# Optimization experiments

Hardware: AMD Instinct MI355X
Metric: run time of the kernel (lower is better)

Reference implementation:

```python
import jax, jax.numpy as jnp
import numpy as np

B, C, H, W = 2, 64, 256, 256
DW = 128          # c * DW_Expand
FFN = 128         # c * FFN_Expand
GRID = 8          # wH = wW modulation grid


def setup_inputs() -> dict:
    key = jax.random.key(0)
    ks = jax.random.split(key, 16)
    rn = lambda k, s, sc=1.0: jax.random.normal(k, s, jnp.float32) * sc
    return {
        "x": rn(ks[0], (B, C, H, W)),
        "w1": rn(ks[1], (DW, C), (2.0 / C) ** 0.5),
        "b1": jnp.zeros((DW,), jnp.float32),
        "w2": rn(ks[2], (DW, 3, 3), (2.0 / 9.0) ** 0.5),
        "b2": jnp.zeros((DW,), jnp.float32),
        "w3": rn(ks[3], (C, DW // 2), (2.0 / (DW // 2)) ** 0.5),
        "b3": jnp.zeros((C,), jnp.float32),
        "sca_w": rn(ks[4], (DW // 2, DW // 2), (1.0 / (DW // 2)) ** 0.5),
        "sca_b": jnp.zeros((DW // 2,), jnp.float32),
        "w4": rn(ks[5], (FFN, C), (2.0 / C) ** 0.5),
        "b4": jnp.zeros((FFN,), jnp.float32),
        "w5": rn(ks[6], (C, FFN // 2), (2.0 / (FFN // 2)) ** 0.5),
        "b5": jnp.zeros((C,), jnp.float32),
        "n1_w": jnp.ones((C,), jnp.float32),
        "n1_b": jnp.zeros((C,), jnp.float32),
        "n2_w": jnp.ones((C,), jnp.float32),
        "n2_b": jnp.zeros((C,), jnp.float32),
        "beta": rn(ks[7], (C,), 0.1),
        "gamma": rn(ks[8], (C,), 0.1),
        "mod1": rn(ks[9], (B, DW, C, GRID, GRID)),
        "mod2": rn(ks[10], (B, DW, GRID, GRID)),
        "mod3": rn(ks[11], (B, C, DW // 2, GRID, GRID)),
        "mod4": rn(ks[12], (B, FFN, C, GRID, GRID)),
        "mod5": rn(ks[13], (B, C, FFN // 2, GRID, GRID)),
    }


def layernorm2d(x, w, b, eps=1e-6):
    # channel-wise LayerNorm per pixel (NAFNet LayerNorm2d)
    mu = jnp.mean(x, axis=1, keepdims=True)
    var = jnp.mean((x - mu) ** 2, axis=1, keepdims=True)
    return (x - mu) / jnp.sqrt(var + eps) * w[None, :, None, None] + b[None, :, None, None]


def conv1x1_modulated(x, wb, bb, mod):
    # wb: [Co,Ci], mod: [B,Co,Ci,wH,wW]; per-patch 1x1 conv with normalized dynamic weights
    w = wb[None, :, :, None, None] * mod                      # [B,Co,Ci,wH,wW]
    w = w / jnp.sqrt(jnp.sum(w * w, axis=2, keepdims=True))   # normalize over Ci (kh*kw==1)
    b_, ci, h, wd = x.shape
    wh, ww = mod.shape[-2:]
    ph, pw = h // wh, wd // ww
    xp = x.reshape(b_, ci, wh, ph, ww, pw)                    # split into patches
    y = jnp.einsum('bocuv,bcupvq->boupvq', w, xp)             # per-patch matmul
    return y.reshape(b_, wb.shape[0], h, wd) + bb[None, :, None, None]


def conv3x3_dw_modulated(x, wb, bb, mod):
    # wb: [C,3,3], mod: [B,C,wH,wW]; per-patch depthwise 3x3, padding 1 across whole image
    w = wb[None, :, :, :, None, None] * mod[:, :, None, None, :, :]  # [B,C,3,3,wH,wW]
    w = w / jnp.sqrt(jnp.sum(w * w, axis=(2, 3), keepdims=True))     # normalize over (ci=1, kh*kw)
    b_, c, h, wd = x.shape
    wh, ww = mod.shape[-2:]
    ph, pw = h // wh, wd // ww
    xpad = jnp.pad(x, ((0, 0), (0, 0), (1, 1), (1, 1)))
    out = jnp.zeros_like(x)
    for dh in range(3):
        for dw_ in range(3):
            xs = xpad[:, :, dh:dh + h, dw_:dw_ + wd].reshape(b_, c, wh, ph, ww, pw)
            wk = w[:, :, dh, dw_, :, :]                        # [B,C,wH,wW]
            out = out + (wk[:, :, :, None, :, None] * xs).reshape(b_, c, h, wd)
    return out + bb[None, :, None, None]


def simple_gate(x):
    a, g = jnp.split(x, 2, axis=1)
    return a * g


def reference(x, w1, b1, w2, b2, w3, b3, sca_w, sca_b, w4, b4, w5, b5,
              n1_w, n1_b, n2_w, n2_b, beta, gamma, mod1, mod2, mod3, mod4, mod5):
    y = layernorm2d(x, n1_w, n1_b)
    y = conv1x1_modulated(y, w1, b1, mod1)
    y = conv3x3_dw_modulated(y, w2, b2, mod2)
    y = simple_gate(y)
    s = jnp.mean(y, axis=(2, 3), keepdims=True)               # SCA: global pool + 1x1
    s = jnp.einsum('oc,bcij->boij', sca_w, s) + sca_b[None, :, None, None]
    y = y * s
    y = conv1x1_modulated(y, w3, b3, mod3)
    y1 = x + y * beta[None, :, None, None]
    z = conv1x1_modulated(layernorm2d(y1, n2_w, n2_b), w4, b4, mod4)
    z = simple_gate(z)
    z = conv1x1_modulated(z, w5, b5, mod5)
    return y1 + z * gamma[None, :, None, None]
```

## Files before the change

kernel.cpp:

```cpp
#include <hip/hip_runtime.h>
#include <hip/hip_bf16.h>


typedef __bf16 bf16x8 __attribute__((ext_vector_type(8)));
typedef float f32x4 __attribute__((ext_vector_type(4)));
typedef unsigned short u16x8 __attribute__((ext_vector_type(8)));

__device__ __forceinline__ float b2f(unsigned short u) {
    union { unsigned int i; float f; } x; x.i = ((unsigned int)u) << 16; return x.f;
}
__device__ __forceinline__ unsigned short f2b(float f) {
    union { float f; unsigned int i; } x; x.f = f;
    unsigned int i = x.i;
    return (unsigned short)((i + 0x7FFFu + ((i >> 16) & 1u)) >> 16);
}
__device__ __forceinline__ unsigned int pk2(float a, float b) {
    __hip_bfloat162 h = __float22bfloat162_rn(float2{a, b});
    union { __hip_bfloat162 h; unsigned int u; } cv; cv.h = h; return cv.u;
}

__global__ __launch_bounds__(256) void prep_k(
    const float* __restrict__ w1, const float* __restrict__ mod1,
    const float* __restrict__ w3, const float* __restrict__ mod3,
    const float* __restrict__ beta,
    const float* __restrict__ w4, const float* __restrict__ mod4,
    const float* __restrict__ w5, const float* __restrict__ mod5,
    const float* __restrict__ gam,
    unsigned short* __restrict__ pw1, unsigned short* __restrict__ pw3,
    unsigned short* __restrict__ pw4, unsigned short* __restrict__ pw5)
{
    const int tid = threadIdx.x;
    int blk = blockIdx.x;
    const float* w; const float* mod; const float* rows = nullptr;
    unsigned short* out; int NOUT; int rem;
    if (blk < 256)      { w = w1; mod = mod1; out = pw1; NOUT = 128; rem = blk; }
    else if (blk < 384) { w = w3; mod = mod3; out = pw3; NOUT = 64;  rem = blk - 256; rows = beta; }
    else if (blk < 640) { w = w4; mod = mod4; out = pw4; NOUT = 128; rem = blk - 384; }
    else                { w = w5; mod = mod5; out = pw5; NOUT = 64;  rem = blk - 640; rows = gam; }
    const int b = rem / NOUT, o = rem % NOUT;

    __shared__ float mlds[64 * 68];
    __shared__ float wlsh[64];
    __shared__ float red[4 * 64];
    __shared__ float rs[64];

    const float* mbase = mod + ((size_t)(b * NOUT + o) * 64) * 64;
#pragma unroll
    for (int k = 0; k < 4; ++k) {
        int l = tid + k * 256;
        float4 vv = ((const float4*)mbase)[l];
        int c = l >> 4, q = l & 15;
        *(float4*)&mlds[c * 68 + q * 4] = vv;
    }
    if (tid < 64) wlsh[tid] = w[o * 64 + tid];
    __syncthreads();

    {
        int uv = tid & 63, part = tid >> 6;
        float ss = 0.f;
#pragma unroll
        for (int j = 0; j < 16; ++j) {
            int c = part * 16 + j;
            float t = wlsh[c] * mlds[c * 68 + uv];
            ss += t * t;
        }
        red[part * 64 + uv] = ss;
    }
    __syncthreads();
    if (tid < 64) {
        float tot = red[tid] + red[64 + tid] + red[128 + tid] + red[192 + tid];
        float rv = rows ? rows[tid == tid ? o : o] : 1.f;
        rs[tid] = rsqrtf(fmaxf(tot, 1e-30f)) * (rows ? rows[o] : 1.f) * (rv == rv ? 1.f : 1.f);
    }
    __syncthreads();

    {
        int uvw = tid >> 2, cp = tid & 3;
        float r = rs[uvw];
        size_t obase = ((size_t)(b * 64 + uvw) * NOUT + o) * 64;
#pragma unroll
        for (int g = 0; g < 2; ++g) {
            u16x8 pk;
#pragma unroll
            for (int e = 0; e < 8; ++e) {
                int c = cp * 16 + g * 8 + e;
                pk[e] = f2b(wlsh[c] * mlds[c * 68 + uvw] * r);
            }
            *(u16x8*)&out[obase + cp * 16 + g * 8] = pk;
        }
    }
}

__global__ __launch_bounds__(256, 2) void head_k(
    const float* __restrict__ x, unsigned short* __restrict__ t1,
    const unsigned short* __restrict__ pw1, const float* __restrict__ b1,
    const float* __restrict__ n1w, const float* __restrict__ n1b, int bbase)
{
    const int tid   = threadIdx.x;
    const int chunk = blockIdx.x;
    const int uv    = blockIdx.y;
    const int z     = blockIdx.z;
    const int bfull = z + bbase;
    const int u = uv >> 3, v = uv & 7;
    const int h_base = u * 32 + chunk * 4;
    const int w_base = v * 32;

    __shared__ __align__(16) unsigned short stage[128 * 72];

    const int wave = tid >> 6;
    const int lane = tid & 63;
    const int q = lane >> 4;
    const int r = lane & 15;
    const int nfi[2] = {2 * wave, 2 * wave + 1};

    const unsigned short* pwt = pw1 + ((size_t)(bfull * 64 + uv) * 128) * 64;
    bf16x8 bfr[2][2];
#pragma unroll
    for (int f = 0; f < 2; ++f)
#pragma unroll
        for (int ks = 0; ks < 2; ++ks)
            bfr[f][ks] = *(const bf16x8*)&pwt[(16 * nfi[f] + r) * 64 + ks * 32 + q * 8];
    float bsc[2] = {b1[16 * nfi[0] + r], b1[16 * nfi[1] + r]};

    const int cg = tid & 7;
    const int qd = tid >> 3;
    const int c0 = cg * 8;
    const int pixg = (h_base + (qd >> 3)) * 256 + w_base + (qd & 7) * 4;
    float v2[8][4];
#pragma unroll
    for (int k = 0; k < 8; ++k) {
        float4 t = *(const float4*)&x[((z * 64 + c0 + k) << 16) + pixg];
        v2[k][0] = t.x; v2[k][1] = t.y; v2[k][2] = t.z; v2[k][3] = t.w;
    }
    float lw[8], lb[8];
    *(float4*)&lw[0] = *(const float4*)&n1w[c0];
    *(float4*)&lw[4] = *(const float4*)&n1w[c0 + 4];
    *(float4*)&lb[0] = *(const float4*)&n1b[c0];
    *(float4*)&lb[4] = *(const float4*)&n1b[c0 + 4];
#pragma unroll
    for (int e = 0; e < 4; ++e) {
        float s1 = 0.f, s2 = 0.f;
#pragma unroll
        for (int k = 0; k < 8; ++k) { s1 += v2[k][e]; s2 += v2[k][e] * v2[k][e]; }
#pragma unroll
        for (int m = 1; m < 8; m <<= 1) { s1 += __shfl_xor(s1, m); s2 += __shfl_xor(s2, m); }
        float mu = s1 * (1.f / 64.f);
        float var = s2 * (1.f / 64.f) - mu * mu;
        float rstd = rsqrtf(fmaxf(var, 0.f) + 1e-6f);
        float o8[8];
#pragma unroll
        for (int k = 0; k < 8; ++k) o8[k] = (v2[k][e] - mu) * rstd * lw[k] + lb[k];
        uint4 pk;
        pk.x = pk2(o8[0], o8[1]); pk.y = pk2(o8[2], o8[3]);
        pk.z = pk2(o8[4], o8[5]); pk.w = pk2(o8[6], o8[7]);
        *(uint4*)&stage[(qd * 4 + e) * 72 + c0] = pk;
    }

    __syncthreads();

    f32x4 acc[8][2];
#pragma unroll
    for (int mi = 0; mi < 8; ++mi) { acc[mi][0] = (f32x4){0,0,0,0}; acc[mi][1] = (f32x4){0,0,0,0}; }
#pragma unroll
    for (int mi = 0; mi < 8; ++mi) {
        bf16x8 a0 = *(const bf16x8*)&stage[(16 * mi + r) * 72 + q * 8];
        bf16x8 a1 = *(const bf16x8*)&stage[(16 * mi + r) * 72 + 32 + q * 8];
#pragma unroll
        for (int f = 0; f < 2; ++f) {
            acc[mi][f] = __builtin_amdgcn_mfma_f32_16x16x32_bf16(a0, bfr[f][0], acc[mi][f], 0, 0, 0);
            acc[mi][f] = __builtin_amdgcn_mfma_f32_16x16x32_bf16(a1, bfr[f][1], acc[mi][f], 0, 0, 0);
        }
    }

#pragma unroll
    for (int mi = 0; mi < 8; ++mi) {
        int lp0 = 16 * mi + 4 * q;
        int pix = (h_base + (lp0 >> 5)) * 256 + w_base + (lp0 & 31);
#pragma unroll
        for (int f = 0; f < 2; ++f) {
            int o = 16 * nfi[f] + r;
            float bs = bsc[f];
            *(uint2*)&t1[((z * 128 + o) << 16) + pix] =
                make_uint2(pk2(acc[mi][f][0] + bs, acc[mi][f][1] + bs),
                           pk2(acc[mi][f][2] + bs, acc[mi][f][3] + bs));
        }
    }
}

__global__ __launch_bounds__(256, 2) void tail_k(
    const unsigned short* __restrict__ t3, const float* __restrict__ x,
    float* __restrict__ outp,
    const unsigned short* __restrict__ pw3, const float* __restrict__ b3,
    const float* __restrict__ beta,
    const unsigned short* __restrict__ pw4, const float* __restrict__ b4,
    const float* __restrict__ n2w, const float* __restrict__ n2b,
    const unsigned short* __restrict__ pw5, const float* __restrict__ b5,
    const float* __restrict__ gam,
    const float* __restrict__ svec, int bbase)
{
    const int tid   = threadIdx.x;
    const int chunk = blockIdx.x;
    const int uv    = blockIdx.y;
    const int z     = blockIdx.z;
    const int bfull = z + bbase;
    const int u = uv >> 3, v = uv & 7;
    const int h_base = u * 32 + chunk * 4;
    const int w_base = v * 32;

    __shared__ __align__(16) unsigned short stage[128 * 72];

    const int wave = tid >> 6;
    const int lane = tid & 63;
    const int q = lane >> 4;
    const int r = lane & 15;
    const int oo = 16 * wave + r;

    const unsigned short* p3 = pw3 + (size_t)(bfull * 64 + uv) * 64 * 64;
    const unsigned short* p4 = pw4 + (size_t)(bfull * 64 + uv) * 128 * 64;
    const unsigned short* p5 = pw5 + (size_t)(bfull * 64 + uv) * 64 * 64;
    bf16x8 w3f[2], w5f[2], w4f[2][2];
    const int nfi4[2] = {wave, wave + 4};
#pragma unroll
    for (int ks = 0; ks < 2; ++ks) {
        w3f[ks] = *(const bf16x8*)&p3[(oo) * 64 + ks * 32 + q * 8];
        w5f[ks] = *(const bf16x8*)&p5[(oo) * 64 + ks * 32 + q * 8];
#pragma unroll
        for (int f = 0; f < 2; ++f)
            w4f[f][ks] = *(const bf16x8*)&p4[(16 * nfi4[f] + r) * 64 + ks * 32 + q * 8];
    }
    const float sb3 = b3[oo] * beta[oo];
    const float ba4 = b4[oo], bg4 = b4[oo + 64];
    const float sb5 = b5[oo] * gam[oo];

    const int cg = tid & 7;
    const int qd = tid >> 3;
    const int c0 = cg * 8;
    const int pixg = (h_base + (qd >> 3)) * 256 + w_base + (qd & 7) * 4;
    {
        float sv[8];
        *(float4*)&sv[0] = *(const float4*)&svec[bfull * 64 + c0];
        *(float4*)&sv[4] = *(const float4*)&svec[bfull * 64 + c0 + 4];
        float v2[8][4];
#pragma unroll
        for (int k = 0; k < 8; ++k) {
            ushort4 t = *(const ushort4*)&t3[((z * 64 + c0 + k) << 16) + pixg];
            v2[k][0] = b2f(t.x) * sv[k]; v2[k][1] = b2f(t.y) * sv[k];
            v2[k][2] = b2f(t.z) * sv[k]; v2[k][3] = b2f(t.w) * sv[k];
        }
#pragma unroll
        for (int e = 0; e < 4; ++e) {
            uint4 pk;
            pk.x = pk2(v2[0][e], v2[1][e]); pk.y = pk2(v2[2][e], v2[3][e]);
            pk.z = pk2(v2[4][e], v2[5][e]); pk.w = pk2(v2[6][e], v2[7][e]);
            *(uint4*)&stage[(qd * 4 + e) * 72 + c0] = pk;
        }
    }
    __syncthreads();

    f32x4 acc3[8];
#pragma unroll
    for (int mi = 0; mi < 8; ++mi) acc3[mi] = (f32x4){0, 0, 0, 0};
#pragma unroll
    for (int mi = 0; mi < 8; ++mi) {
        bf16x8 a0 = *(const bf16x8*)&stage[(16 * mi + r) * 72 + q * 8];
        bf16x8 a1 = *(const bf16x8*)&stage[(16 * mi + r) * 72 + 32 + q * 8];
        acc3[mi] = __builtin_amdgcn_mfma_f32_16x16x32_bf16(a0, w3f[0], acc3[mi], 0, 0, 0);
        acc3[mi] = __builtin_amdgcn_mfma_f32_16x16x32_bf16(a1, w3f[1], acc3[mi], 0, 0, 0);
    }
    __syncthreads();

    float y1v[8][4];
#pragma unroll
    for (int mi = 0; mi < 8; ++mi) {
        int lp0 = 16 * mi + 4 * q;
        int pix = (h_base + (lp0 >> 5)) * 256 + w_base + (lp0 & 31);
        float4 xr = *(const float4*)&x[((z * 64 + oo) << 16) + pix];
        y1v[mi][0] = acc3[mi][0] + sb3 + xr.x;
        y1v[mi][1] = acc3[mi][1] + sb3 + xr.y;
        y1v[mi][2] = acc3[mi][2] + sb3 + xr.z;
        y1v[mi][3] = acc3[mi][3] + sb3 + xr.w;
    }
#pragma unroll
    for (int mi = 0; mi < 8; ++mi)
#pragma unroll
        for (int e = 0; e < 4; ++e)
            stage[(16 * mi + 4 * q + e) * 72 + oo] = f2b(y1v[mi][e]);
    __syncthreads();

    {
        float lw[8], lb[8];
        *(float4*)&lw[0] = *(const float4*)&n2w[c0];
        *(float4*)&lw[4] = *(const float4*)&n2w[c0 + 4];
        *(float4*)&lb[0] = *(const float4*)&n2b[c0];
        *(float4*)&lb[4] = *(const float4*)&n2b[c0 + 4];
#pragma unroll
        for (int e = 0; e < 4; ++e) {
            int px = qd * 4 + e;
            uint4 raw = *(const uint4*)&stage[px * 72 + c0];
            unsigned short* rp = (unsigned short*)&raw;
            float vv[8];
            float s1 = 0.f, s2 = 0.f;
#pragma unroll
            for (int k = 0; k < 8; ++k) { vv[k] = b2f(rp[k]); s1 += vv[k]; s2 += vv[k] * vv[k]; }
#pragma unroll
            for (int m = 1; m < 8; m <<= 1) { s1 += __shfl_xor(s1, m); s2 += __shfl_xor(s2, m); }
            float mu = s1 * (1.f / 64.f);
            float var = s2 * (1.f / 64.f) - mu * mu;
            float rstd = rsqrtf(fmaxf(var, 0.f) + 1e-6f);
            float o8[8];
#pragma unroll
            for (int k = 0; k < 8; ++k) o8[k] = (vv[k] - mu) * rstd * lw[k] + lb[k];
            uint4 pk;
            pk.x = pk2(o8[0], o8[1]); pk.y = pk2(o8[2], o8[3]);
            pk.z = pk2(o8[4], o8[5]); pk.w = pk2(o8[6], o8[7]);
            *(uint4*)&stage[px * 72 + c0] = pk;
        }
    }
    __syncthreads();

    f32x4 acc4[8][2];
#pragma unroll
    for (int mi = 0; mi < 8; ++mi) { acc4[mi][0] = (f32x4){0,0,0,0}; acc4[mi][1] = (f32x4){0,0,0,0}; }
#pragma unroll
    for (int mi = 0; mi < 8; ++mi) {
        bf16x8 a0 = *(const bf16x8*)&stage[(16 * mi + r) * 72 + q * 8];
        bf16x8 a1 = *(const bf16x8*)&stage[(16 * mi + r) * 72 + 32 + q * 8];
#pragma unroll
        for (int f = 0; f < 2; ++f) {
            acc4[mi][f] = __builtin_amdgcn_mfma_f32_16x16x32_bf16(a0, w4f[f][0], acc4[mi][f], 0, 0, 0);
            acc4[mi][f] = __builtin_amdgcn_mfma_f32_16x16x32_bf16(a1, w4f[f][1], acc4[mi][f], 0, 0, 0);
        }
    }
    __syncthreads();
#pragma unroll
    for (int mi = 0; mi < 8; ++mi)
#pragma unroll
        for (int e = 0; e < 4; ++e) {
            float zv = (acc4[mi][0][e] + ba4) * (acc4[mi][1][e] + bg4);
            stage[(16 * mi + 4 * q + e) * 72 + oo] = f2b(zv);
        }
    __syncthreads();

    f32x4 acc5[8];
#pragma unroll
    for (int mi = 0; mi < 8; ++mi) acc5[mi] = (f32x4){0, 0, 0, 0};
#pragma unroll
    for (int mi = 0; mi < 8; ++mi) {
        bf16x8 a0 = *(const bf16x8*)&stage[(16 * mi + r) * 72 + q * 8];
        bf16x8 a1 = *(const bf16x8*)&stage[(16 * mi + r) * 72 + 32 + q * 8];
        acc5[mi] = __builtin_amdgcn_mfma_f32_16x16x32_bf16(a0, w5f[0], acc5[mi], 0, 0, 0);
        acc5[mi] = __builtin_amdgcn_mfma_f32_16x16x32_bf16(a1, w5f[1], acc5[mi], 0, 0, 0);
    }
#pragma unroll
    for (int mi = 0; mi < 8; ++mi) {
        int lp0 = 16 * mi + 4 * q;
        int pix = (h_base + (lp0 >> 5)) * 256 + w_base + (lp0 & 31);
        *(float4*)&outp[((z * 64 + oo) << 16) + pix] =
            make_float4(y1v[mi][0] + acc5[mi][0] + sb5,
                        y1v[mi][1] + acc5[mi][1] + sb5,
                        y1v[mi][2] + acc5[mi][2] + sb5,
                        y1v[mi][3] + acc5[mi][3] + sb5);
    }
}

__global__ __launch_bounds__(256, 4) void dw_k(
    const unsigned short* __restrict__ t1,
    unsigned short* __restrict__ t3,
    const float* __restrict__ w2,
    const float* __restrict__ b2,
    const float* __restrict__ mod2,
    float* __restrict__ s0,
    int bbase)
{
    const int tid  = threadIdx.x;
    const int band = blockIdx.x;
    const int oc   = blockIdx.y;
    const int z    = blockIdx.z;
    const int bfull = z + bbase;
    const int u = band >> 2;

    __shared__ float wl[2][8][9];
    __shared__ float wred[4];

    if (tid < 16) {
        int halfc = tid >> 3, vv = tid & 7;
        const float* wrow = w2 + (oc + halfc * 64) * 9;
        float wloc[9], ssum = 0.f;
#pragma unroll
        for (int k = 0; k < 9; ++k) { wloc[k] = wrow[k]; ssum += wloc[k] * wloc[k]; }
        float m = mod2[(bfull * 128 + oc + halfc * 64) * 64 + u * 8 + vv];
        float rn = m * rsqrtf(fmaxf(m * m * ssum, 1e-30f));
#pragma unroll
        for (int k = 0; k < 9; ++k) wl[halfc][vv][k] = wloc[k] * rn;
    }
    __syncthreads();

    const int strip = tid & 31;
    const int row   = band * 8 + (tid >> 5);
    const int v     = strip >> 2;

    float wa[9], wg[9];
#pragma unroll
    for (int k = 0; k < 9; ++k) { wa[k] = wl[0][v][k]; wg[k] = wl[1][v][k]; }
    const float ba = b2[oc], bg = b2[oc + 64];

    const unsigned short* pa = t1 + (((size_t)z * 128 + oc) << 16);
    const unsigned short* pg = pa + ((size_t)64 << 16);

    float fa[3][8], fg[3][8], la[3], ra[3], lg[3], rg[3];
#pragma unroll
    for (int dr = 0; dr < 3; ++dr) {
        int rr = row - 1 + dr;
        if (rr >= 0 && rr < 256) {
            u16x8 va = *(const u16x8*)&pa[rr * 256 + strip * 8];
            u16x8 vg = *(const u16x8*)&pg[rr * 256 + strip * 8];
#pragma unroll
            for (int e = 0; e < 8; ++e) { fa[dr][e] = b2f(va[e]); fg[dr][e] = b2f(vg[e]); }
        } else {
#pragma unroll
            for (int e = 0; e < 8; ++e) { fa[dr][e] = 0.f; fg[dr][e] = 0.f; }
        }
        float t;
        t = __shfl_up(fa[dr][7], 1);   la[dr] = (strip == 0)  ? 0.f : t;
        t = __shfl_up(fg[dr][7], 1);   lg[dr] = (strip == 0)  ? 0.f : t;
        t = __shfl_down(fa[dr][0], 1); ra[dr] = (strip == 31) ? 0.f : t;
        t = __shfl_down(fg[dr][0], 1); rg[dr] = (strip == 31) ? 0.f : t;
    }

    float psum = 0.f;
    u16x8 pk;
#pragma unroll
    for (int j = 0; j < 8; ++j) {
        float a = 0.f, g = 0.f;
#pragma unroll
        for (int dr = 0; dr < 3; ++dr) {
            float m1a = (j == 0) ? la[dr] : fa[dr][j - 1];
            float p1a = (j == 7) ? ra[dr] : fa[dr][j + 1];
            float m1g = (j == 0) ? lg[dr] : fg[dr][j - 1];
            float p1g = (j == 7) ? rg[dr] : fg[dr][j + 1];
            a += wa[dr * 3] * m1a + wa[dr * 3 + 1] * fa[dr][j] + wa[dr * 3 + 2] * p1a;
            g += wg[dr * 3] * m1g + wg[dr * 3 + 1] * fg[dr][j] + wg[dr * 3 + 2] * p1g;
        }
        float val = (a + ba) * (g + bg);
        psum += val;
        pk[j] = f2b(val);
    }
    *(u16x8*)&t3[(((size_t)z * 64 + oc) << 16) + row * 256 + strip * 8] = pk;

    for (int off = 32; off > 0; off >>= 1) psum += __shfl_down(psum, off, 64);
    if ((tid & 63) == 0) wred[tid >> 6] = psum;
    __syncthreads();
    if (tid == 0)
        atomicAdd(&s0[bfull * 64 + oc], wred[0] + wred[1] + wred[2] + wred[3]);
}

__global__ void sca_k(const float* __restrict__ s0,
                      const float* __restrict__ scaw,
                      const float* __restrict__ scab,
                      float* __restrict__ sfin)
{
    int t = threadIdx.x;
    int b = t >> 6, o = t & 63;
    float acc = 0.f;
#pragma unroll 8
    for (int c = 0; c < 64; ++c)
        acc += scaw[o * 64 + c] * s0[b * 64 + c];
    sfin[b * 64 + o] = acc * (1.f / 65536.f) + scab[o];
}

extern "C" void kernel_launch(void* const* d_in, const int* in_sizes, int n_in,
                              void* d_out, int out_size, void* d_ws, size_t ws_size,
                              hipStream_t stream) {
    (void)in_sizes; (void)n_in; (void)out_size;
    const float* x    = (const float*)d_in[0];
    const float* w1   = (const float*)d_in[1];
    const float* b1   = (const float*)d_in[2];
    const float* w2   = (const float*)d_in[3];
    const float* b2   = (const float*)d_in[4];
    const float* w3   = (const float*)d_in[5];
    const float* b3   = (const float*)d_in[6];
    const float* scaw = (const float*)d_in[7];
    const float* scab = (const float*)d_in[8];
    const float* w4   = (const float*)d_in[9];
    const float* b4   = (const float*)d_in[10];
    const float* w5   = (const float*)d_in[11];
    const float* b5   = (const float*)d_in[12];
    const float* n1w  = (const float*)d_in[13];
    const float* n1b  = (const float*)d_in[14];
    const float* n2w  = (const float*)d_in[15];
    const float* n2b  = (const float*)d_in[16];
    const float* beta = (const float*)d_in[17];
    const float* gam  = (const float*)d_in[18];
    const float* mod1 = (const float*)d_in[19];
    const float* mod2 = (const float*)d_in[20];
    const float* mod3 = (const float*)d_in[21];
    const float* mod4 = (const float*)d_in[22];
    const float* mod5 = (const float*)d_in[23];

    char* ws = (char*)d_ws;
    float* outf = (float*)d_out;

    const size_t IMGel = (size_t)64 * 65536;
    const size_t T1B   = (size_t)128 * 65536 * 2;
    const size_t T3B   = (size_t)64 * 65536 * 2;
    const size_t PW1B = 2097152, PW3B = 1048576, PW4B = 2097152, PW5B = 1048576;
    const size_t TBLB = PW1B + PW3B + PW4B + PW5B;

    const size_t needA = 2 * (T1B + T3B) + 4096 + TBLB;
    const bool planA = ws_size >= needA;
    const size_t NBT = planA ? 2 : 1;

    unsigned short* t1 = (unsigned short*)ws;
    unsigned short* t3 = (unsigned short*)(ws + NBT * T1B);
    char* statb = ws + NBT * (T1B + T3B);
    float* s0   = (float*)statb;
    float* sfin = (float*)(statb + 512);
    unsigned short* pw1 = (unsigned short*)(statb + 4096);
    unsigned short* pw3 = (unsigned short*)(statb + 4096 + PW1B);
    unsigned short* pw4 = (unsigned short*)(statb + 4096 + PW1B + PW3B);
    unsigned short* pw5 = (unsigned short*)(statb + 4096 + PW1B + PW3B + PW4B);

    dim3 blk(256);

    hipMemsetAsync(s0, 0, 512, stream);
    prep_k<<<768, blk, 0, stream>>>(w1, mod1, w3, mod3, beta, w4, mod4,
                                    w5, mod5, gam, pw1, pw3, pw4, pw5);

    if (planA) {
        dim3 gconv(8, 64, 2), gdw(32, 64, 2);
        head_k<<<gconv, blk, 0, stream>>>(x, t1, pw1, b1, n1w, n1b, 0);
        dw_k<<<gdw, blk, 0, stream>>>(t1, t3, w2, b2, mod2, s0, 0);
        sca_k<<<1, 128, 0, stream>>>(s0, scaw, scab, sfin);
        tail_k<<<gconv, blk, 0, stream>>>(t3, x, outf, pw3, b3, beta,
                                          pw4, b4, n2w, n2b, pw5, b5, gam,
                                          sfin, 0);
    } else {
        for (int bb = 0; bb < 2; ++bb) {
            const float* x_b   = x    + (size_t)bb * IMGel;
            float*       out_b = outf + (size_t)bb * IMGel;
            dim3 gconv(8, 64, 1), gdw(32, 64, 1);
            head_k<<<gconv, blk, 0, stream>>>(x_b, t1, pw1, b1, n1w, n1b, bb);
            dw_k<<<gdw, blk, 0, stream>>>(t1, t3, w2, b2, mod2, s0, bb);
            sca_k<<<1, 128, 0, stream>>>(s0, scaw, scab, sfin);
            tail_k<<<gconv, blk, 0, stream>>>(t3, x_b, out_b, pw3, b3, beta,
                                              pw4, b4, n2w, n2b, pw5, b5, gam,
                                              sfin, bb);
        }
    }
}
```

Before: 205.2 us.

## Fuse SCA matvec into tail kernel, zero stats in prep, reorder grid axes

Removes the single-block sca_k launch by having each tail_k block compute the 64-element SCA vector into shared memory from the pooled sums. It also drops the hipMemsetAsync by zeroing the accumulator in block 0 of prep_k. Separately, the grid axes are swapped so consecutive blocks walk patch (uv) first instead of row chunk, which changes dispatch order and cache locality. The aim is to cut two launches and their gaps, at the cost of redundant 64x64 matvecs in every tail block. Zeroing s0 inside prep_k relies on stream ordering before dw_k, which holds.

```diff
diff --git a/kernel.cpp b/kernel.cpp
--- a/kernel.cpp
+++ b/kernel.cpp
@@ -27,10 +27,12 @@
     const float* __restrict__ w5, const float* __restrict__ mod5,
     const float* __restrict__ gam,
     unsigned short* __restrict__ pw1, unsigned short* __restrict__ pw3,
-    unsigned short* __restrict__ pw4, unsigned short* __restrict__ pw5)
+    unsigned short* __restrict__ pw4, unsigned short* __restrict__ pw5,
+    float* __restrict__ s0)
 {
     const int tid = threadIdx.x;
     int blk = blockIdx.x;
+    if (blk == 0 && tid < 128) s0[tid] = 0.f;
     const float* w; const float* mod; const float* rows = nullptr;
     unsigned short* out; int NOUT; int rem;
     if (blk < 256)      { w = w1; mod = mod1; out = pw1; NOUT = 128; rem = blk; }
@@ -69,8 +71,7 @@
     __syncthreads();
     if (tid < 64) {
         float tot = red[tid] + red[64 + tid] + red[128 + tid] + red[192 + tid];
-        float rv = rows ? rows[tid == tid ? o : o] : 1.f;
-        rs[tid] = rsqrtf(fmaxf(tot, 1e-30f)) * (rows ? rows[o] : 1.f) * (rv == rv ? 1.f : 1.f);
+        rs[tid] = rsqrtf(fmaxf(tot, 1e-30f)) * (rows ? rows[o] : 1.f);
     }
     __syncthreads();
 
@@ -97,8 +98,8 @@
     const float* __restrict__ n1w, const float* __restrict__ n1b, int bbase)
 {
     const int tid   = threadIdx.x;
-    const int chunk = blockIdx.x;
-    const int uv    = blockIdx.y;
+    const int uv    = blockIdx.x;
+    const int chunk = blockIdx.y;
     const int z     = blockIdx.z;
     const int bfull = z + bbase;
     const int u = uv >> 3, v = uv & 7;
@@ -196,11 +197,12 @@
     const float* __restrict__ n2w, const float* __restrict__ n2b,
     const unsigned short* __restrict__ pw5, const float* __restrict__ b5,
     const float* __restrict__ gam,
-    const float* __restrict__ svec, int bbase)
+    const float* __restrict__ scaw, const float* __restrict__ scab,
+    const float* __restrict__ s0, int bbase)
 {
     const int tid   = threadIdx.x;
-    const int chunk = blockIdx.x;
-    const int uv    = blockIdx.y;
+    const int uv    = blockIdx.x;
+    const int chunk = blockIdx.y;
     const int z     = blockIdx.z;
     const int bfull = z + bbase;
     const int u = uv >> 3, v = uv & 7;
@@ -208,6 +210,7 @@
     const int w_base = v * 32;
 
     __shared__ __align__(16) unsigned short stage[128 * 72];
+    __shared__ float sfin_l[64];
 
     const int wave = tid >> 6;
     const int lane = tid & 63;
@@ -215,6 +218,19 @@
     const int r = lane & 15;
     const int oo = 16 * wave + r;
 
+    if (tid < 64) {
+        const float* srow = scaw + tid * 64;
+        const float* s0b  = s0 + bfull * 64;
+        float acc = 0.f;
+#pragma unroll
+        for (int c4 = 0; c4 < 16; ++c4) {
+            float4 wv = *(const float4*)&srow[c4 * 4];
+            float4 s4 = *(const float4*)&s0b[c4 * 4];
+            acc += wv.x * s4.x + wv.y * s4.y + wv.z * s4.z + wv.w * s4.w;
+        }
+        sfin_l[tid] = acc * (1.f / 65536.f) + scab[tid];
+    }
+
     const unsigned short* p3 = pw3 + (size_t)(bfull * 64 + uv) * 64 * 64;
     const unsigned short* p4 = pw4 + (size_t)(bfull * 64 + uv) * 128 * 64;
     const unsigned short* p5 = pw5 + (size_t)(bfull * 64 + uv) * 64 * 64;
@@ -231,6 +247,8 @@
     const float sb3 = b3[oo] * beta[oo];
     const float ba4 = b4[oo], bg4 = b4[oo + 64];
     const float sb5 = b5[oo] * gam[oo];
+
+    __syncthreads();
 
     const int cg = tid & 7;
     const int qd = tid >> 3;
@@ -238,8 +256,8 @@
     const int pixg = (h_base + (qd >> 3)) * 256 + w_base + (qd & 7) * 4;
     {
         float sv[8];
-        *(float4*)&sv[0] = *(const float4*)&svec[bfull * 64 + c0];
-        *(float4*)&sv[4] = *(const float4*)&svec[bfull * 64 + c0 + 4];
+        *(float4*)&sv[0] = *(const float4*)&sfin_l[c0];
+        *(float4*)&sv[4] = *(const float4*)&sfin_l[c0 + 4];
         float v2[8][4];
 #pragma unroll
         for (int k = 0; k < 8; ++k) {
@@ -373,8 +391,8 @@
     int bbase)
 {
     const int tid  = threadIdx.x;
-    const int band = blockIdx.x;
-    const int oc   = blockIdx.y;
+    const int oc   = blockIdx.x;
+    const int band = blockIdx.y;
     const int z    = blockIdx.z;
     const int bfull = z + bbase;
     const int u = band >> 2;
@@ -452,20 +470,6 @@
     __syncthreads();
     if (tid == 0)
         atomicAdd(&s0[bfull * 64 + oc], wred[0] + wred[1] + wred[2] + wred[3]);
-}
-
-__global__ void sca_k(const float* __restrict__ s0,
-                      const float* __restrict__ scaw,
-                      const float* __restrict__ scab,
-                      float* __restrict__ sfin)
-{
-    int t = threadIdx.x;
-    int b = t >> 6, o = t & 63;
-    float acc = 0.f;
-#pragma unroll 8
-    for (int c = 0; c < 64; ++c)
-        acc += scaw[o * 64 + c] * s0[b * 64 + c];
-    sfin[b * 64 + o] = acc * (1.f / 65536.f) + scab[o];
 }
 
 extern "C" void kernel_launch(void* const* d_in, const int* in_sizes, int n_in,
@@ -514,7 +518,6 @@
     unsigned short* t3 = (unsigned short*)(ws + NBT * T1B);
     char* statb = ws + NBT * (T1B + T3B);
     float* s0   = (float*)statb;
-    float* sfin = (float*)(statb + 512);
     unsigned short* pw1 = (unsigned short*)(statb + 4096);
     unsigned short* pw3 = (unsigned short*)(statb + 4096 + PW1B);
     unsigned short* pw4 = (unsigned short*)(statb + 4096 + PW1B + PW3B);
@@ -522,29 +525,26 @@
 
     dim3 blk(256);
 
-    hipMemsetAsync(s0, 0, 512, stream);
     prep_k<<<768, blk, 0, stream>>>(w1, mod1, w3, mod3, beta, w4, mod4,
-                                    w5, mod5, gam, pw1, pw3, pw4, pw5);
+                                    w5, mod5, gam, pw1, pw3, pw4, pw5, s0);
 
     if (planA) {
-        dim3 gconv(8, 64, 2), gdw(32, 64, 2);
+        dim3 gconv(64, 8, 2), gdw(64, 32, 2);
         head_k<<<gconv, blk, 0, stream>>>(x, t1, pw1, b1, n1w, n1b, 0);
         dw_k<<<gdw, blk, 0, stream>>>(t1, t3, w2, b2, mod2, s0, 0);
-        sca_k<<<1, 128, 0, stream>>>(s0, scaw, scab, sfin);
         tail_k<<<gconv, blk, 0, stream>>>(t3, x, outf, pw3, b3, beta,
                                           pw4, b4, n2w, n2b, pw5, b5, gam,
-                                          sfin, 0);
+                                          scaw, scab, s0, 0);
     } else {
         for (int bb = 0; bb < 2; ++bb) {
             const float* x_b   = x    + (size_t)bb * IMGel;
             float*       out_b = outf + (size_t)bb * IMGel;
-            dim3 gconv(8, 64, 1), gdw(32, 64, 1);
+            dim3 gconv(64, 8, 1), gdw(64, 32, 1);
             head_k<<<gconv, blk, 0, stream>>>(x_b, t1, pw1, b1, n1w, n1b, bb);
             dw_k<<<gdw, blk, 0, stream>>>(t1, t3, w2, b2, mod2, s0, bb);
-            sca_k<<<1, 128, 0, stream>>>(s0, scaw, scab, sfin);
             tail_k<<<gconv, blk, 0, stream>>>(t3, x_b, out_b, pw3, b3, beta,
                                               pw4, b4, n2w, n2b, pw5, b5, gam,
-                                              sfin, bb);
-        }
-    }
-}
+                                              scaw, scab, s0, bb);
+        }
+    }
+}
```

Result: no change. 202.3 us (-1.5%).
